# Performance work log

Hardware: AMD Instinct MI355X
Metric: run time of the kernel (lower is better)

The kernel has to match this reference:

```python
import math
import jax, jax.numpy as jnp
import numpy as np

T = 100        # temporal_scale
N = 32         # num_sample
PERBIN = 3     # num_sample_perbin
RATIO = 0.5    # prop_boundary_ratio
FEAT = 400     # feat_dim
B = 4          # batch


def _make_sample_mask(tscale=T, ratio=RATIO, n=N, perbin=PERBIN):
    # mask[t, sample_idx, start_idx, end_idx], faithful to _get_sample_mask
    mask = np.zeros((tscale, n, tscale, tscale), dtype=np.float64)
    for end_i in range(tscale):
        for start_i in range(end_i + 1):
            sp, ep = float(start_i), float(end_i + 1)
            L = ep - sp + 1.0
            sp2 = sp - L * ratio
            ep2 = ep + L * ratio
            step = (ep2 - sp2) / (n * perbin - 1.0)
            samples = [sp2 + step * i for i in range(n * perbin)]
            for i in range(n):
                for j in samples[i * perbin:(i + 1) * perbin]:
                    fr, it = math.modf(j)
                    it = int(it)
                    if 0 <= it < tscale - 1:
                        mask[it, i, start_i, end_i] += (1.0 - fr) / perbin
                        mask[it + 1, i, start_i, end_i] += fr / perbin
    return mask.reshape(tscale, -1).astype(np.float32)  # [T, N*T*T]


_DN = {1: ('NCH', 'OIH', 'NCH'), 2: ('NCHW', 'OIHW', 'NCHW'), 3: ('NCDHW', 'OIDHW', 'NCDHW')}


def _conv(x, w, b, stride, padding, groups=1):
    nd = x.ndim - 2
    if isinstance(stride, int):
        stride = (stride,) * nd
    if isinstance(padding, int):
        padding = [(padding, padding)] * nd
    y = jax.lax.conv_general_dilated(x, w, stride, padding,
                                     dimension_numbers=_DN[nd],
                                     feature_group_count=groups)
    return y + b.reshape((1, -1) + (1,) * nd)


def _forward(inputs, w_b1, b_b1, w_b2, b_b2, w_s1, b_s1, w_s2, b_s2,
             w_e1, b_e1, w_e2, b_e2, w_p1, b_p1, w3d, b3d,
             w2a, b2a, w2b, b2b, w2c, b2c, w2d, b2d, sample_mask):
    relu, sig = jax.nn.relu, jax.nn.sigmoid
    base = relu(_conv(inputs, w_b1, b_b1, 1, 1, 4))
    base = relu(_conv(base, w_b2, b_b2, 1, 1, 4))           # [B,256,T]
    start = sig(_conv(relu(_conv(base, w_s1, b_s1, 1, 1, 4)), w_s2, b_s2, 1, 0))[:, 0]
    end = sig(_conv(relu(_conv(base, w_e1, b_e1, 1, 1, 4)), w_e2, b_e2, 1, 0))[:, 0]
    p = relu(_conv(base, w_p1, b_p1, 1, 1))                 # [B,128,T]
    Bsz, C, Tt = p.shape
    n = w3d.shape[2]
    # boundary-matching layer: [B,128,T] @ [T, N*T*T] -> [B,128,N,T,T]
    bm = jnp.matmul(p, sample_mask).reshape(Bsz, C, n, Tt, Tt)
    bm = relu(_conv(bm, w3d, b3d, (n, 1, 1), 0))[:, :, 0]   # [B,512,T,T]
    x = relu(_conv(bm, w2a, b2a, 1, 0))
    x = relu(_conv(x, w2b, b2b, 1, 1))
    x = relu(_conv(x, w2c, b2c, 1, 1))
    conf = sig(_conv(x, w2d, b2d, 1, 0))                     # [B,2,T,T]
    return conf, start, end


def setup_inputs() -> dict:
    key = jax.random.key(0)
    ks = iter(jax.random.split(key, 40))

    def rn(shape, s=0.05):
        return jax.random.normal(next(ks), shape, jnp.float32) * s

    d = dict(
        inputs=jax.random.normal(next(ks), (B, FEAT, T), jnp.float32),
        w_b1=rn((256, FEAT // 4, 3)), b_b1=rn((256,)),
        w_b2=rn((256, 64, 3)), b_b2=rn((256,)),
        w_s1=rn((256, 64, 3)), b_s1=rn((256,)),
        w_s2=rn((1, 256, 1)), b_s2=rn((1,)),
        w_e1=rn((256, 64, 3)), b_e1=rn((256,)),
        w_e2=rn((1, 256, 1)), b_e2=rn((1,)),
        w_p1=rn((128, 256, 3)), b_p1=rn((128,)),
        w3d=rn((512, 128, N, 1, 1)), b3d=rn((512,)),
        w2a=rn((128, 512, 1, 1)), b2a=rn((128,)),
        w2b=rn((128, 128, 3, 3)), b2b=rn((128,)),
        w2c=rn((128, 128, 3, 3)), b2c=rn((128,)),
        w2d=rn((2, 128, 1, 1)), b2d=rn((2,)),
        sample_mask=jnp.asarray(_make_sample_mask()),
    )
    return d


def reference(inputs, w_b1, b_b1, w_b2, b_b2, w_s1, b_s1, w_s2, b_s2,
              w_e1, b_e1, w_e2, b_e2, w_p1, b_p1, w3d, b3d,
              w2a, b2a, w2b, b2b, w2c, b2c, w2d, b2d, sample_mask):
    return _forward(inputs, w_b1, b_b1, w_b2, b_b2, w_s1, b_s1, w_s2, b_s2,
                    w_e1, b_e1, w_e2, b_e2, w_p1, b_p1, w3d, b3d,
                    w2a, b2a, w2b, b2b, w2c, b2c, w2d, b2d, sample_mask)
```

## Files before the change

### kernel.cpp

```cpp
#include <hip/hip_runtime.h>
#include <cstdint>
#include <cstddef>
#include <math.h>

typedef unsigned short u16;
typedef short bf16x8 __attribute__((ext_vector_type(8)));
typedef float f32x4 __attribute__((ext_vector_type(4)));

__device__ __forceinline__ u16 f2bf(float f) {
  union { float f; uint32_t u; } c; c.f = f;
  uint32_t u = c.u;
  return (u16)((u + 0x7FFFu + ((u >> 16) & 1u)) >> 16);
}
__device__ __forceinline__ float bf2f(u16 h) {
  union { uint32_t u; float f; } c; c.u = ((uint32_t)h) << 16;
  return c.f;
}
__device__ __forceinline__ float sigmoidf_(float x) { return 1.f / (1.f + expf(-x)); }

__device__ __forceinline__ void glds16(const void* g, void* l) {
  __builtin_amdgcn_global_load_lds((const __attribute__((address_space(1))) void*)g,
                                   (__attribute__((address_space(3))) void*)l, 16, 0, 0);
}

__device__ __forceinline__ int col_rank(int p) {
  int s = p / 100, e = p - s * 100;
  int tri = (s * (s - 1)) >> 1;
  return (e >= s) ? (p - tri - s) : (5050 + tri + e);
}

__global__ void conv1d_k3v(const float* __restrict__ in, const float* __restrict__ w,
                           const float* __restrict__ bias, float* __restrict__ out,
                           int Cin_total, int Cin_g, int ocPerGroup, int OC) {
  int idx = blockIdx.x * 256 + threadIdx.x;
  int sub = idx % 25;
  int tmp = idx / 25;
  int oc = tmp % OC;
  int bb = tmp / OC;
  if (bb >= 4) return;
  int t4 = sub * 4;
  int g = oc / ocPerGroup;
  const float* ip = in + ((size_t)bb * Cin_total + (size_t)g * Cin_g) * 100 + t4;
  const float* wp = w + (size_t)oc * Cin_g * 3;
  float bs = bias[oc];
  float s0 = bs, s1 = bs, s2 = bs, s3 = bs;
  #pragma unroll 4
  for (int ic = 0; ic < Cin_g; ++ic) {
    const float* r = ip + (size_t)ic * 100;
    float4 a = *(const float4*)r;
    float xm = (t4 > 0) ? r[-1] : 0.f;
    float xp = (t4 < 96) ? r[4] : 0.f;
    float w0 = wp[ic * 3 + 0], w1 = wp[ic * 3 + 1], w2 = wp[ic * 3 + 2];
    s0 += w0 * xm + w1 * a.x + w2 * a.y;
    s1 += w0 * a.x + w1 * a.y + w2 * a.z;
    s2 += w0 * a.y + w1 * a.z + w2 * a.w;
    s3 += w0 * a.z + w1 * a.w + w2 * xp;
  }
  float4 o;
  o.x = fmaxf(s0, 0.f); o.y = fmaxf(s1, 0.f);
  o.z = fmaxf(s2, 0.f); o.w = fmaxf(s3, 0.f);
  *(float4*)(out + ((size_t)bb * OC + oc) * 100 + t4) = o;
}

__global__ void conv1d_branch_v(const float* __restrict__ in, const float* __restrict__ wS,
                                const float* __restrict__ bS, const float* __restrict__ wE,
                                const float* __restrict__ bE, const float* __restrict__ wP,
                                const float* __restrict__ bP, float* __restrict__ outS,
                                float* __restrict__ outE, u16* __restrict__ Pt) {
  int idx = blockIdx.x * 256 + threadIdx.x;
  int sub = idx % 25;
  int tmp = idx / 25;
  int ocx = tmp % 640;
  int bb = tmp / 640;
  if (bb >= 4) return;
  int t4 = sub * 4;
  const float* w;
  const float* bias;
  const float* ip;
  int Cin_g, oc;
  if (ocx < 512) {
    int sel = ocx >> 8;
    oc = ocx & 255;
    w = sel ? wE : wS;
    bias = sel ? bE : bS;
    int g = oc >> 6;
    ip = in + ((size_t)bb * 256 + (size_t)g * 64) * 100 + t4;
    Cin_g = 64;
  } else {
    oc = ocx - 512;
    w = wP;
    bias = bP;
    ip = in + (size_t)bb * 256 * 100 + t4;
    Cin_g = 256;
  }
  const float* wp = w + (size_t)oc * Cin_g * 3;
  float bs = bias[oc];
  float s0 = bs, s1 = bs, s2 = bs, s3 = bs;
  #pragma unroll 4
  for (int ic = 0; ic < Cin_g; ++ic) {
    const float* r = ip + (size_t)ic * 100;
    float4 a = *(const float4*)r;
    float xm = (t4 > 0) ? r[-1] : 0.f;
    float xp = (t4 < 96) ? r[4] : 0.f;
    float w0 = wp[ic * 3 + 0], w1 = wp[ic * 3 + 1], w2 = wp[ic * 3 + 2];
    s0 += w0 * xm + w1 * a.x + w2 * a.y;
    s1 += w0 * a.x + w1 * a.y + w2 * a.z;
    s2 += w0 * a.y + w1 * a.z + w2 * a.w;
    s3 += w0 * a.z + w1 * a.w + w2 * xp;
  }
  if (ocx < 512) {
    float* out = (ocx < 256) ? outS : outE;
    float4 o;
    o.x = fmaxf(s0, 0.f); o.y = fmaxf(s1, 0.f);
    o.z = fmaxf(s2, 0.f); o.w = fmaxf(s3, 0.f);
    *(float4*)(out + ((size_t)bb * 256 + oc) * 100 + t4) = o;
  } else {
    Pt[((size_t)bb * 100 + t4 + 0) * 128 + oc] = f2bf(fmaxf(s0, 0.f));
    Pt[((size_t)bb * 100 + t4 + 1) * 128 + oc] = f2bf(fmaxf(s1, 0.f));
    Pt[((size_t)bb * 100 + t4 + 2) * 128 + oc] = f2bf(fmaxf(s2, 0.f));
    Pt[((size_t)bb * 100 + t4 + 3) * 128 + oc] = f2bf(fmaxf(s3, 0.f));
  }
}

__global__ void prep_fused(const float* __restrict__ w2a, const float* __restrict__ w2b,
                           const float* __restrict__ w2c, u16* __restrict__ w2a_bf,
                           u16* __restrict__ w2b_pk, u16* __restrict__ w2c_pk,
                           const float* __restrict__ w3d, u16* __restrict__ Wq,
                           int* __restrict__ invperm, int* __restrict__ tinfo,
                           int* __restrict__ order, u16* __restrict__ zp,
                           u16* __restrict__ Mt, const float* __restrict__ inputs,
                           const float* __restrict__ w_b1, const float* __restrict__ b_b1,
                           float* __restrict__ base1) {
  __shared__ __align__(16) u16 ML[4 * 3200];
  __shared__ int C[128];
  int bid = blockIdx.x, tid = threadIdx.x;
  if (bid < 576) {
    int i = bid * 256 + tid;
    if (i < 65536) w2a_bf[i] = f2bf(w2a[i]);
    if (i < 147456) {
      int oc = i / 1152, r = i % 1152, kk = r >> 7, ic = r & 127;
      int src = (oc * 128 + ic) * 9 + kk;
      w2b_pk[i] = f2bf(w2b[src]);
      w2c_pk[i] = f2bf(w2c[src]);
    }
  } else if (bid < 640) {
    int u = (bid - 576) * 256 + tid;
    int o = u >> 5, n = u & 31;
    const float* src = w3d + (size_t)o * 4096 + n;
    u16* dst = Wq + (size_t)u * 128;
    for (int c0 = 0; c0 < 128; c0 += 8) {
      __align__(16) u16 h[8];
      #pragma unroll
      for (int j = 0; j < 8; ++j) h[j] = f2bf(src[(size_t)(c0 + j) * 32]);
      *(uint4*)(dst + c0) = *(const uint4*)h;
    }
  } else if (bid < 680) {
    int p = (bid - 640) * 256 + tid;
    if (p < 10000) invperm[col_rank(p)] = p;
  } else if (bid == 680) {
    if (tid < 128) zp[tid] = 0;
    int t = tid;
    int kbmin = 0, cnt = 0;
    if (t < 79) {
      int rlo = t * 128;
      int rhi = rlo + 128;
      if (rhi > 5050) rhi = 5050;
      if (rlo < 5050) {
        int s = 0;
        while (100 * (s + 1) - ((s + 1) * s) / 2 <= rlo) ++s;
        int cum = 100 * s - (s * (s - 1)) / 2;
        int tmin = 100, tmax = -1;
        for (int r = rlo; r < rhi; ++r) {
          while (r - cum >= 100 - s) { ++s; cum = 100 * s - (s * (s - 1)) / 2; }
          int e = s + (r - cum);
          float L = (float)(e - s + 2);
          float sp2 = (float)s - 0.5f * L;
          float ep2 = (float)(e + 1) + 0.5f * L;
          int a = (int)floorf(sp2) - 1;
          if (a < 0) a = 0;
          int b = (int)floorf(ep2) + 2;
          if (b > 99) b = 99;
          if (a < tmin) tmin = a;
          if (b > tmax) tmax = b;
        }
        kbmin = tmin >> 1;
        cnt = (tmax >> 1) - kbmin + 1;
      }
      tinfo[2 * t] = kbmin;
      tinfo[2 * t + 1] = cnt;
    }
    if (t < 128) C[t] = (t < 79) ? cnt : -1;
    __syncthreads();
    if (t < 79) {
      int pos = 0;
      int ct = C[t];
      for (int u = 0; u < 79; ++u) {
        int cu = C[u];
        pos += (cu > ct) || (cu == ct && u < t);
      }
      order[pos] = t;
    }
  } else if (bid < 1961) {
    int r0 = (bid - 681) * 4;
    uint32_t* MZ = (uint32_t*)ML;
    for (int i = tid; i < 6400; i += 256) MZ[i] = 0;
    __syncthreads();
    int g = tid >> 6, lane = tid & 63;
    int r = r0 + g;
    if (r < 5050 && lane < 32) {
      int n = lane;
      int s = (int)((201.0 - sqrt((double)(40401 - 8 * r))) * 0.5);
      if (s < 0) s = 0;
      while (s * (201 - s) / 2 > r) --s;
      while ((s + 1) * (200 - s) / 2 <= r) ++s;
      int e = s + (r - s * (201 - s) / 2);
      double sp = (double)s, ep = (double)(e + 1);
      double L = ep - sp + 1.0;
      double sp2 = sp - L * 0.5;
      double ep2 = ep + L * 0.5;
      double step = (ep2 - sp2) / 95.0;
      double win[8];
      #pragma unroll
      for (int k = 0; k < 8; ++k) win[k] = 0.0;
      int base = -1;
      #pragma unroll
      for (int jj = 0; jj < 3; ++jj) {
        double pos = sp2 + step * (double)(n * 3 + jj);
        double ip;
        double fr = modf(pos, &ip);
        int it = (int)ip;
        if (it >= 0 && it < 99) {
          if (base < 0) base = it;
          int off = it - base;
          win[off] += (1.0 - fr) / 3.0;
          win[off + 1] += fr / 3.0;
        }
      }
      if (base >= 0) {
        u16* dst = ML + g * 3200 + n;
        #pragma unroll
        for (int k = 0; k < 8; ++k) {
          int t = base + k;
          if (t < 100) dst[t * 32] = f2bf((float)win[k]);
        }
      }
    }
    __syncthreads();
    for (int i = tid; i < 1600; i += 256) {
      int rl = i / 400, off = i - rl * 400;
      *(uint4*)(Mt + (size_t)(r0 + rl) * 3200 + off * 8) = ((const uint4*)ML)[i];
    }
  } else {
    int idx = (bid - 1961) * 256 + tid;
    int sub = idx % 25;
    int tmp = idx / 25;
    int oc = tmp % 256;
    int bb = tmp / 256;
    if (bb >= 4) return;
    int t4 = sub * 4;
    int g = oc >> 6;
    const float* ip = inputs + ((size_t)bb * 400 + (size_t)g * 100) * 100 + t4;
    const float* wp = w_b1 + (size_t)oc * 300;
    float bs = b_b1[oc];
    float s0 = bs, s1 = bs, s2 = bs, s3 = bs;
    #pragma unroll 4
    for (int ic = 0; ic < 100; ++ic) {
      const float* rr = ip + (size_t)ic * 100;
      float4 a = *(const float4*)rr;
      float xm = (t4 > 0) ? rr[-1] : 0.f;
      float xp = (t4 < 96) ? rr[4] : 0.f;
      float w0 = wp[ic * 3 + 0], w1 = wp[ic * 3 + 1], w2 = wp[ic * 3 + 2];
      s0 += w0 * xm + w1 * a.x + w2 * a.y;
      s1 += w0 * a.x + w1 * a.y + w2 * a.z;
      s2 += w0 * a.y + w1 * a.z + w2 * a.w;
      s3 += w0 * a.z + w1 * a.w + w2 * xp;
    }
    float4 o;
    o.x = fmaxf(s0, 0.f); o.y = fmaxf(s1, 0.f);
    o.z = fmaxf(s2, 0.f); o.w = fmaxf(s3, 0.f);
    *(float4*)(base1 + ((size_t)bb * 256 + oc) * 100 + t4) = o;
  }
}

template<int MI>
__device__ __forceinline__ void mfma_stepT(const u16* As, const u16* Bs, int l, int wm, int wn,
                                           f32x4 (&acc)[MI][4]) {
  int m15 = l & 15, q = l >> 4, sw = m15 & 7;
  #pragma unroll
  for (int kk = 0; kk < 2; ++kk) {
    int koff = ((kk * 4 + q) ^ sw) * 8;
    bf16x8 av[MI], bv[4];
    #pragma unroll
    for (int i = 0; i < MI; ++i)
      av[i] = *(const bf16x8*)(As + (size_t)(wm * (MI * 16) + i * 16 + m15) * 64 + koff);
    #pragma unroll
    for (int j = 0; j < 4; ++j)
      bv[j] = *(const bf16x8*)(Bs + (size_t)(wn * 64 + j * 16 + m15) * 64 + koff);
    #pragma unroll
    for (int i = 0; i < MI; ++i) {
      #pragma unroll
      for (int j = 0; j < 4; ++j)
        acc[i][j] = __builtin_amdgcn_mfma_f32_16x16x32_bf16(av[i], bv[j], acc[i][j], 0, 0, 0);
    }
  }
}

template<int MI>
__device__ __forceinline__ void epilogue_storeT(f32x4 (&acc)[MI][4], u16* OUT,
                                                const float* bias, int row0, int col0, int l,
                                                int wm, int wn, int N, int OC, long long NPB,
                                                const int* colmap) {
  int r4 = (l >> 4) * 4, c1 = l & 15;
  int cols[4], pcols[4];
  #pragma unroll
  for (int j = 0; j < 4; ++j) {
    cols[j] = col0 + wn * 64 + j * 16 + c1;
    pcols[j] = (cols[j] < N) ? (colmap ? colmap[cols[j]] : cols[j]) : 0;
  }
  #pragma unroll
  for (int i = 0; i < MI; ++i) {
    int row = row0 + wm * (MI * 16) + i * 16 + r4;
    int ob = row % OC;
    size_t obb = (size_t)(row / OC) * (size_t)OC * (size_t)NPB;
    float b0 = bias[ob + 0], b1 = bias[ob + 1], b2 = bias[ob + 2], b3 = bias[ob + 3];
    #pragma unroll
    for (int j = 0; j < 4; ++j) {
      if (cols[j] < N) {
        f32x4 v = acc[i][j];
        __align__(8) u16 h[4];
        h[0] = f2bf(fmaxf(v[0] + b0, 0.f));
        h[1] = f2bf(fmaxf(v[1] + b1, 0.f));
        h[2] = f2bf(fmaxf(v[2] + b2, 0.f));
        h[3] = f2bf(fmaxf(v[3] + b3, 0.f));
        *(uint2*)(OUT + obb + (size_t)pcols[j] * OC + ob) = *(const uint2*)h;
      }
    }
  }
}

__global__ __launch_bounds__(256, 2) void gemm_bt(const u16* __restrict__ A,
                                                  const u16* __restrict__ B,
                                                  u16* __restrict__ OUT,
                                                  const float* __restrict__ bias, int N, int K,
                                                  const int* __restrict__ tinfo,
                                                  const int* __restrict__ order, int kblocks,
                                                  int OC, long long NPB, int NclampB,
                                                  const int* __restrict__ colmap) {
  __shared__ __align__(16) u16 As[128 * 64];
  __shared__ __align__(16) u16 Bs[128 * 64];
  int mt = blockIdx.x;
  int nt = order ? order[blockIdx.y] : blockIdx.y;
  int col0 = nt * 128, row0 = mt * 128;
  int tid = threadIdx.x, w = tid >> 6, l = tid & 63;
  int wm = w >> 1, wn = w & 1;
  int lr = l >> 3;
  int lk_sw = ((l & 7) ^ lr) * 8;
  f32x4 acc[4][4] = {};
  size_t aoff[4];
  size_t boff[4];
  #pragma unroll
  for (int r = 0; r < 4; ++r) {
    int chunk = r * 4 + w;
    int rowA = row0 + chunk * 8 + lr;
    aoff[r] = (size_t)rowA * K + lk_sw;
    int colB = col0 + chunk * 8 + lr;
    if (colB >= NclampB) colB = NclampB - 1;
    boff[r] = (size_t)colB * K + lk_sw;
  }
  int kbmin = 0, cnt = kblocks;
  if (tinfo) { kbmin = tinfo[2 * nt]; cnt = tinfo[2 * nt + 1]; }
  for (int i = 0; i < cnt; ++i) {
    int k0 = (kbmin + i) * 64;
    #pragma unroll
    for (int r = 0; r < 4; ++r) {
      int chunk = r * 4 + w;
      glds16(A + aoff[r] + k0, As + chunk * 512);
      glds16(B + boff[r] + k0, Bs + chunk * 512);
    }
    __syncthreads();
    mfma_stepT<4>(As, Bs, l, wm, wn, acc);
    __syncthreads();
  }
  epilogue_storeT<4>(acc, OUT, bias, row0, col0, l, wm, wn, N, OC, NPB, colmap);
}

__global__ __launch_bounds__(256, 2) void qprep_sig(const u16* __restrict__ Wq,
                                                    const u16* __restrict__ Pt,
                                                    u16* __restrict__ Qb,
                                                    const float* __restrict__ s1,
                                                    const float* __restrict__ e1,
                                                    const float* __restrict__ ws2,
                                                    const float* __restrict__ bs2,
                                                    const float* __restrict__ we2,
                                                    const float* __restrict__ be2,
                                                    float* __restrict__ out) {
  if (blockIdx.x == 128) {
    int t = threadIdx.x & 127;
    int sel = threadIdx.x >> 7;
    int bb = blockIdx.y;
    if (t >= 100) return;
    const float* in = sel ? e1 : s1;
    const float* w = sel ? we2 : ws2;
    float s = sel ? be2[0] : bs2[0];
    #pragma unroll 8
    for (int c = 0; c < 256; ++c) s += w[c] * in[((size_t)bb * 256 + c) * 100 + t];
    out[80000 + sel * 400 + bb * 100 + t] = sigmoidf_(s);
    return;
  }
  __shared__ __align__(16) u16 As[128 * 64];
  __shared__ __align__(16) u16 Bs[128 * 64];
  int mt = blockIdx.x, nt = blockIdx.y;
  int col0 = nt * 128, row0 = mt * 128;
  int tid = threadIdx.x, w = tid >> 6, l = tid & 63;
  int wm = w >> 1, wn = w & 1;
  int lr = l >> 3;
  int lk_sw = ((l & 7) ^ lr) * 8;
  f32x4 acc[4][4] = {};
  size_t aoff[4];
  size_t boff[4];
  #pragma unroll
  for (int r = 0; r < 4; ++r) {
    int chunk = r * 4 + w;
    int rowA = row0 + chunk * 8 + lr;
    aoff[r] = (size_t)rowA * 128 + lk_sw;
    int colB = col0 + chunk * 8 + lr;
    if (colB >= 400) colB = 399;
    boff[r] = (size_t)colB * 128 + lk_sw;
  }
  #pragma unroll
  for (int kb = 0; kb < 2; ++kb) {
    int k0 = kb * 64;
    #pragma unroll
    for (int r = 0; r < 4; ++r) {
      int chunk = r * 4 + w;
      glds16(Wq + aoff[r] + k0, As + chunk * 512);
      glds16(Pt + boff[r] + k0, Bs + chunk * 512);
    }
    __syncthreads();
    mfma_stepT<4>(As, Bs, l, wm, wn, acc);
    __syncthreads();
  }
  int r4 = (l >> 4) * 4, c1 = l & 15;
  #pragma unroll
  for (int i = 0; i < 4; ++i) {
    int row = row0 + wm * 64 + i * 16 + r4;
    int o = row >> 5, n = row & 31;
    #pragma unroll
    for (int j = 0; j < 4; ++j) {
      int col = col0 + wn * 64 + j * 16 + c1;
      if (col < 400) {
        int b = col / 100, t = col - b * 100;
        f32x4 v = acc[i][j];
        __align__(8) u16 h[4];
        h[0] = f2bf(v[0]);
        h[1] = f2bf(v[1]);
        h[2] = f2bf(v[2]);
        h[3] = f2bf(v[3]);
        *(uint2*)(Qb + ((size_t)(b * 512 + o)) * 3200 + t * 32 + n) = *(const uint2*)h;
      }
    }
  }
}

template<int FUSE>
__global__ __launch_bounds__(256, 2) void conv3x3_gemm(const u16* __restrict__ Apk,
                                                       const u16* __restrict__ X,
                                                       u16* __restrict__ OUT,
                                                       const float* __restrict__ bias,
                                                       const u16* __restrict__ zp,
                                                       const float* __restrict__ w2d,
                                                       const float* __restrict__ b2d,
                                                       float* __restrict__ out) {
  __shared__ __align__(16) u16 SH[2 * 128 * 64];
  u16* As = SH;
  u16* Bs = SH + 128 * 64;
  int nt = blockIdx.x;
  int col0 = nt * 128;
  int tid = threadIdx.x, w = tid >> 6, l = tid & 63;
  int wm = w >> 1, wn = w & 1;
  int lr = l >> 3;
  int lk_sw = ((l & 7) ^ lr) * 8;
  int cj[4], yy[4], xx[4];
  bool vv[4];
  size_t aoff[4];
  #pragma unroll
  for (int r = 0; r < 4; ++r) {
    int chunk = r * 4 + w;
    int c = col0 + chunk * 8 + lr;
    cj[r] = c;
    vv[r] = (c < 40000);
    int p = c % 10000;
    yy[r] = p / 100;
    xx[r] = p % 100;
    aoff[r] = (size_t)(chunk * 8 + lr) * 1152 + lk_sw;
  }
  f32x4 acc[4][4] = {};
  for (int s = 0; s < 9; ++s) {
    int dy = s / 3 - 1, dx = s % 3 - 1;
    int doff = dy * 100 + dx;
    #pragma unroll
    for (int half = 0; half < 2; ++half) {
      int k0 = s * 128 + half * 64;
      int c0 = half * 64;
      #pragma unroll
      for (int r = 0; r < 4; ++r) {
        int chunk = r * 4 + w;
        glds16(Apk + aoff[r] + k0, As + chunk * 512);
        int y2 = yy[r] + dy, x2 = xx[r] + dx;
        bool ok = vv[r] && ((unsigned)y2 < 100u) && ((unsigned)x2 < 100u);
        const u16* src = ok ? (X + (size_t)(cj[r] + doff) * 128 + c0 + lk_sw) : zp;
        glds16(src, Bs + chunk * 512);
      }
      __syncthreads();
      mfma_stepT<4>(As, Bs, l, wm, wn, acc);
      __syncthreads();
    }
  }
  if (FUSE == 0) {
    epilogue_storeT<4>(acc, OUT, bias, 0, col0, l, wm, wn, 40000, 128, 40000LL, nullptr);
  } else {
    uint32_t* W = (uint32_t*)SH;
    int r4 = (l >> 4) * 4, c1 = l & 15;
    #pragma unroll
    for (int i = 0; i < 4; ++i) {
      int ob = wm * 64 + i * 16 + r4;
      float b0 = bias[ob + 0], b1 = bias[ob + 1], b2 = bias[ob + 2], b3 = bias[ob + 3];
      #pragma unroll
      for (int j = 0; j < 4; ++j) {
        int col = wn * 64 + j * 16 + c1;
        f32x4 v = acc[i][j];
        uint32_t lo = (uint32_t)f2bf(fmaxf(v[0] + b0, 0.f)) |
                      ((uint32_t)f2bf(fmaxf(v[1] + b1, 0.f)) << 16);
        uint32_t hi = (uint32_t)f2bf(fmaxf(v[2] + b2, 0.f)) |
                      ((uint32_t)f2bf(fmaxf(v[3] + b3, 0.f)) << 16);
        int jj = ob >> 1;
        W[col * 64 + (jj ^ (col & 31))] = lo;
        W[col * 64 + ((jj + 1) ^ (col & 31))] = hi;
      }
    }
    __syncthreads();
    int col = tid & 127, sel = tid >> 7;
    int gcol = col0 + col;
    if (gcol < 40000) {
      float sum = b2d[sel];
      const uint32_t* Wc = W + col * 64;
      const float* wd = w2d + sel * 128;
      #pragma unroll 8
      for (int c = 0; c < 64; ++c) {
        uint32_t v = Wc[c ^ (col & 31)];
        sum += wd[2 * c] * bf2f((u16)(v & 0xffffu)) + wd[2 * c + 1] * bf2f((u16)(v >> 16));
      }
      int b = gcol / 10000, pidx = gcol - b * 10000;
      out[((size_t)b * 2 + sel) * 10000 + pidx] = sigmoidf_(sum);
    }
  }
}

extern "C" void kernel_launch(void* const* d_in, const int* in_sizes, int n_in, void* d_out,
                              int out_size, void* d_ws, size_t ws_size, hipStream_t stream) {
  const float* inputs = (const float*)d_in[0];
  const float* w_b1 = (const float*)d_in[1];
  const float* b_b1 = (const float*)d_in[2];
  const float* w_b2 = (const float*)d_in[3];
  const float* b_b2 = (const float*)d_in[4];
  const float* w_s1 = (const float*)d_in[5];
  const float* b_s1 = (const float*)d_in[6];
  const float* w_s2 = (const float*)d_in[7];
  const float* b_s2 = (const float*)d_in[8];
  const float* w_e1 = (const float*)d_in[9];
  const float* b_e1 = (const float*)d_in[10];
  const float* w_e2 = (const float*)d_in[11];
  const float* b_e2 = (const float*)d_in[12];
  const float* w_p1 = (const float*)d_in[13];
  const float* b_p1 = (const float*)d_in[14];
  const float* w3d = (const float*)d_in[15];
  const float* b3d = (const float*)d_in[16];
  const float* w2a = (const float*)d_in[17];
  const float* b2a = (const float*)d_in[18];
  const float* w2b = (const float*)d_in[19];
  const float* b2b = (const float*)d_in[20];
  const float* w2c = (const float*)d_in[21];
  const float* b2c = (const float*)d_in[22];
  const float* w2d = (const float*)d_in[23];
  const float* b2d = (const float*)d_in[24];
  float* out = (float*)d_out;
  char* ws = (char*)d_ws;

  int* tinfo = (int*)(ws + 0);
  int* order = (int*)(ws + 2048);
  u16* zp = (u16*)(ws + 16384);
  int* invperm = (int*)(ws + 45056);
  float* base1 = (float*)(ws + 90112);
  float* base = (float*)(ws + 499712);
  float* s1buf = (float*)(ws + 909312);
  u16* Pt = (u16*)(ws + 1318912);
  u16* w2a_bf = (u16*)(ws + 1421312);
  u16* w2b_pk = (u16*)(ws + 1552384);
  u16* w2c_pk = (u16*)(ws + 1847296);
  u16* Qb = (u16*)(ws + 2142208);
  u16* Mt = (u16*)(ws + 15249408);
  float* e1buf = (float*)(ws + 48017408);
  u16* C1t = (u16*)(ws + 79249408);
  u16* Wq = (u16*)(ws + 79249408);
  u16* x2t = Qb;
  u16* x3t = C1t;

  prep_fused<<<2061, 256, 0, stream>>>(w2a, w2b, w2c, w2a_bf, w2b_pk, w2c_pk, w3d, Wq,
                                       invperm, tinfo, order, zp, Mt, inputs, w_b1, b_b1,
                                       base1);

  conv1d_k3v<<<100, 256, 0, stream>>>(base1, w_b2, b_b2, base, 256, 64, 64, 256);
  conv1d_branch_v<<<250, 256, 0, stream>>>(base, w_s1, b_s1, w_e1, b_e1, w_p1, b_p1,
                                           s1buf, e1buf, Pt);

  qprep_sig<<<dim3(129, 4), 256, 0, stream>>>(Wq, Pt, Qb, s1buf, e1buf, w_s2, b_s2,
                                              w_e2, b_e2, out);

  gemm_bt<<<dim3(16, 79), 256, 0, stream>>>(Qb, Mt, C1t, b3d, 10000, 3200, tinfo, order, 50,
                                            512, 10000LL, 10000, invperm);
  gemm_bt<<<dim3(1, 313), 256, 0, stream>>>(w2a_bf, C1t, x2t, b2a, 40000, 512, nullptr,
                                            nullptr, 8, 128, 40000LL, 40000, nullptr);
  conv3x3_gemm<0><<<dim3(313), 256, 0, stream>>>(w2b_pk, x2t, x3t, b2b, zp, nullptr, nullptr,
                                                 nullptr);
  conv3x3_gemm<1><<<dim3(313), 256, 0, stream>>>(w2c_pk, x3t, nullptr, b2c, zp, w2d, b2d,
                                                 out);
}
```

Measured before the change: 257.4 us.

## Split conv1d input channels across 4 lanes and coalesce GEMM epilogue stores via LDS

The three 1D conv kernels now split each output's input-channel reduction across 4 adjacent lanes and combine the partial sums with xor shuffles. This gives 4x more threads and shorter serial loops, raising parallelism for these small, latency-bound kernels. Separately, the GEMM and conv3x3 epilogue now stage bf16 results in shared memory and write each output column as contiguous 16-byte stores instead of scattered 8-byte stores. The costs are an extra __syncthreads, LDS traffic and shuffle reductions.

```diff
diff --git a/kernel.cpp b/kernel.cpp
--- a/kernel.cpp
+++ b/kernel.cpp
@@ -29,96 +29,105 @@
   return (e >= s) ? (p - tri - s) : (5050 + tri + e);
 }
 
-__global__ void conv1d_k3v(const float* __restrict__ in, const float* __restrict__ w,
-                           const float* __restrict__ bias, float* __restrict__ out,
-                           int Cin_total, int Cin_g, int ocPerGroup, int OC) {
-  int idx = blockIdx.x * 256 + threadIdx.x;
-  int sub = idx % 25;
-  int tmp = idx / 25;
-  int oc = tmp % OC;
-  int bb = tmp / OC;
-  if (bb >= 4) return;
+__global__ void conv2_r(const float* __restrict__ in, const float* __restrict__ w,
+                        const float* __restrict__ bias, float* __restrict__ out) {
+  int u = blockIdx.x * 256 + threadIdx.x;
+  int r = u & 3;
+  int quad = u >> 2;
+  int sub = quad % 25;
+  int tmp = quad / 25;
+  int oc = tmp & 255;
+  int bb = tmp >> 8;
   int t4 = sub * 4;
-  int g = oc / ocPerGroup;
-  const float* ip = in + ((size_t)bb * Cin_total + (size_t)g * Cin_g) * 100 + t4;
-  const float* wp = w + (size_t)oc * Cin_g * 3;
-  float bs = bias[oc];
-  float s0 = bs, s1 = bs, s2 = bs, s3 = bs;
+  int g = oc >> 6;
+  const float* ip = in + ((size_t)bb * 256 + g * 64 + r * 16) * 100 + t4;
+  const float* wp = w + (size_t)oc * 192 + r * 48;
+  float s0 = 0.f, s1 = 0.f, s2 = 0.f, s3 = 0.f;
   #pragma unroll 4
-  for (int ic = 0; ic < Cin_g; ++ic) {
-    const float* r = ip + (size_t)ic * 100;
-    float4 a = *(const float4*)r;
-    float xm = (t4 > 0) ? r[-1] : 0.f;
-    float xp = (t4 < 96) ? r[4] : 0.f;
-    float w0 = wp[ic * 3 + 0], w1 = wp[ic * 3 + 1], w2 = wp[ic * 3 + 2];
+  for (int i = 0; i < 16; ++i) {
+    const float* rr = ip + (size_t)i * 100;
+    float4 a = *(const float4*)rr;
+    float xm = (t4 > 0) ? rr[-1] : 0.f;
+    float xp = (t4 < 96) ? rr[4] : 0.f;
+    float w0 = wp[i * 3 + 0], w1 = wp[i * 3 + 1], w2 = wp[i * 3 + 2];
     s0 += w0 * xm + w1 * a.x + w2 * a.y;
     s1 += w0 * a.x + w1 * a.y + w2 * a.z;
     s2 += w0 * a.y + w1 * a.z + w2 * a.w;
     s3 += w0 * a.z + w1 * a.w + w2 * xp;
   }
-  float4 o;
-  o.x = fmaxf(s0, 0.f); o.y = fmaxf(s1, 0.f);
-  o.z = fmaxf(s2, 0.f); o.w = fmaxf(s3, 0.f);
-  *(float4*)(out + ((size_t)bb * OC + oc) * 100 + t4) = o;
-}
-
-__global__ void conv1d_branch_v(const float* __restrict__ in, const float* __restrict__ wS,
-                                const float* __restrict__ bS, const float* __restrict__ wE,
-                                const float* __restrict__ bE, const float* __restrict__ wP,
-                                const float* __restrict__ bP, float* __restrict__ outS,
-                                float* __restrict__ outE, u16* __restrict__ Pt) {
-  int idx = blockIdx.x * 256 + threadIdx.x;
-  int sub = idx % 25;
-  int tmp = idx / 25;
+  s0 += __shfl_xor(s0, 1); s0 += __shfl_xor(s0, 2);
+  s1 += __shfl_xor(s1, 1); s1 += __shfl_xor(s1, 2);
+  s2 += __shfl_xor(s2, 1); s2 += __shfl_xor(s2, 2);
+  s3 += __shfl_xor(s3, 1); s3 += __shfl_xor(s3, 2);
+  if (r == 0) {
+    float b = bias[oc];
+    float4 o;
+    o.x = fmaxf(s0 + b, 0.f); o.y = fmaxf(s1 + b, 0.f);
+    o.z = fmaxf(s2 + b, 0.f); o.w = fmaxf(s3 + b, 0.f);
+    *(float4*)(out + ((size_t)bb * 256 + oc) * 100 + t4) = o;
+  }
+}
+
+__global__ void branch_r(const float* __restrict__ in, const float* __restrict__ wS,
+                         const float* __restrict__ bS, const float* __restrict__ wE,
+                         const float* __restrict__ bE, const float* __restrict__ wP,
+                         const float* __restrict__ bP, float* __restrict__ outS,
+                         float* __restrict__ outE, u16* __restrict__ Pt) {
+  int u = blockIdx.x * 256 + threadIdx.x;
+  int r = u & 3;
+  int quad = u >> 2;
+  int sub = quad % 25;
+  int tmp = quad / 25;
   int ocx = tmp % 640;
   int bb = tmp / 640;
-  if (bb >= 4) return;
   int t4 = sub * 4;
-  const float* w;
-  const float* bias;
+  const float* wp;
   const float* ip;
-  int Cin_g, oc;
+  int oc, iters;
   if (ocx < 512) {
     int sel = ocx >> 8;
     oc = ocx & 255;
-    w = sel ? wE : wS;
-    bias = sel ? bE : bS;
+    wp = (sel ? wE : wS) + (size_t)oc * 192 + r * 48;
     int g = oc >> 6;
-    ip = in + ((size_t)bb * 256 + (size_t)g * 64) * 100 + t4;
-    Cin_g = 64;
+    ip = in + ((size_t)bb * 256 + g * 64 + r * 16) * 100 + t4;
+    iters = 16;
   } else {
     oc = ocx - 512;
-    w = wP;
-    bias = bP;
-    ip = in + (size_t)bb * 256 * 100 + t4;
-    Cin_g = 256;
-  }
-  const float* wp = w + (size_t)oc * Cin_g * 3;
-  float bs = bias[oc];
-  float s0 = bs, s1 = bs, s2 = bs, s3 = bs;
-  #pragma unroll 4
-  for (int ic = 0; ic < Cin_g; ++ic) {
-    const float* r = ip + (size_t)ic * 100;
-    float4 a = *(const float4*)r;
-    float xm = (t4 > 0) ? r[-1] : 0.f;
-    float xp = (t4 < 96) ? r[4] : 0.f;
-    float w0 = wp[ic * 3 + 0], w1 = wp[ic * 3 + 1], w2 = wp[ic * 3 + 2];
+    wp = wP + (size_t)oc * 768 + r * 192;
+    ip = in + ((size_t)bb * 256 + r * 64) * 100 + t4;
+    iters = 64;
+  }
+  float s0 = 0.f, s1 = 0.f, s2 = 0.f, s3 = 0.f;
+  for (int i = 0; i < iters; ++i) {
+    const float* rr = ip + (size_t)i * 100;
+    float4 a = *(const float4*)rr;
+    float xm = (t4 > 0) ? rr[-1] : 0.f;
+    float xp = (t4 < 96) ? rr[4] : 0.f;
+    float w0 = wp[i * 3 + 0], w1 = wp[i * 3 + 1], w2 = wp[i * 3 + 2];
     s0 += w0 * xm + w1 * a.x + w2 * a.y;
     s1 += w0 * a.x + w1 * a.y + w2 * a.z;
     s2 += w0 * a.y + w1 * a.z + w2 * a.w;
     s3 += w0 * a.z + w1 * a.w + w2 * xp;
   }
-  if (ocx < 512) {
-    float* out = (ocx < 256) ? outS : outE;
-    float4 o;
-    o.x = fmaxf(s0, 0.f); o.y = fmaxf(s1, 0.f);
-    o.z = fmaxf(s2, 0.f); o.w = fmaxf(s3, 0.f);
-    *(float4*)(out + ((size_t)bb * 256 + oc) * 100 + t4) = o;
-  } else {
-    Pt[((size_t)bb * 100 + t4 + 0) * 128 + oc] = f2bf(fmaxf(s0, 0.f));
-    Pt[((size_t)bb * 100 + t4 + 1) * 128 + oc] = f2bf(fmaxf(s1, 0.f));
-    Pt[((size_t)bb * 100 + t4 + 2) * 128 + oc] = f2bf(fmaxf(s2, 0.f));
-    Pt[((size_t)bb * 100 + t4 + 3) * 128 + oc] = f2bf(fmaxf(s3, 0.f));
+  s0 += __shfl_xor(s0, 1); s0 += __shfl_xor(s0, 2);
+  s1 += __shfl_xor(s1, 1); s1 += __shfl_xor(s1, 2);
+  s2 += __shfl_xor(s2, 1); s2 += __shfl_xor(s2, 2);
+  s3 += __shfl_xor(s3, 1); s3 += __shfl_xor(s3, 2);
+  if (r == 0) {
+    if (ocx < 512) {
+      float b = (ocx < 256) ? bS[oc] : bE[oc];
+      float* out = (ocx < 256) ? outS : outE;
+      float4 o;
+      o.x = fmaxf(s0 + b, 0.f); o.y = fmaxf(s1 + b, 0.f);
+      o.z = fmaxf(s2 + b, 0.f); o.w = fmaxf(s3 + b, 0.f);
+      *(float4*)(out + ((size_t)bb * 256 + oc) * 100 + t4) = o;
+    } else {
+      float b = bP[oc];
+      Pt[((size_t)bb * 100 + t4 + 0) * 128 + oc] = f2bf(fmaxf(s0 + b, 0.f));
+      Pt[((size_t)bb * 100 + t4 + 1) * 128 + oc] = f2bf(fmaxf(s1 + b, 0.f));
+      Pt[((size_t)bb * 100 + t4 + 2) * 128 + oc] = f2bf(fmaxf(s2 + b, 0.f));
+      Pt[((size_t)bb * 100 + t4 + 3) * 128 + oc] = f2bf(fmaxf(s3 + b, 0.f));
+    }
   }
 }
 
@@ -251,34 +260,41 @@
       *(uint4*)(Mt + (size_t)(r0 + rl) * 3200 + off * 8) = ((const uint4*)ML)[i];
     }
   } else {
-    int idx = (bid - 1961) * 256 + tid;
-    int sub = idx % 25;
-    int tmp = idx / 25;
-    int oc = tmp % 256;
-    int bb = tmp / 256;
-    if (bb >= 4) return;
+    int u = (bid - 1961) * 256 + tid;
+    int r = u & 3;
+    int quad = u >> 2;
+    int sub = quad % 25;
+    int tmp = quad / 25;
+    int oc = tmp & 255;
+    int bb = tmp >> 8;
     int t4 = sub * 4;
     int g = oc >> 6;
-    const float* ip = inputs + ((size_t)bb * 400 + (size_t)g * 100) * 100 + t4;
-    const float* wp = w_b1 + (size_t)oc * 300;
-    float bs = b_b1[oc];
-    float s0 = bs, s1 = bs, s2 = bs, s3 = bs;
-    #pragma unroll 4
-    for (int ic = 0; ic < 100; ++ic) {
-      const float* rr = ip + (size_t)ic * 100;
+    const float* ip = inputs + ((size_t)bb * 400 + g * 100 + r * 25) * 100 + t4;
+    const float* wp = w_b1 + (size_t)oc * 300 + r * 75;
+    float s0 = 0.f, s1 = 0.f, s2 = 0.f, s3 = 0.f;
+    #pragma unroll 5
+    for (int i = 0; i < 25; ++i) {
+      const float* rr = ip + (size_t)i * 100;
       float4 a = *(const float4*)rr;
       float xm = (t4 > 0) ? rr[-1] : 0.f;
       float xp = (t4 < 96) ? rr[4] : 0.f;
-      float w0 = wp[ic * 3 + 0], w1 = wp[ic * 3 + 1], w2 = wp[ic * 3 + 2];
+      float w0 = wp[i * 3 + 0], w1 = wp[i * 3 + 1], w2 = wp[i * 3 + 2];
       s0 += w0 * xm + w1 * a.x + w2 * a.y;
       s1 += w0 * a.x + w1 * a.y + w2 * a.z;
       s2 += w0 * a.y + w1 * a.z + w2 * a.w;
       s3 += w0 * a.z + w1 * a.w + w2 * xp;
     }
-    float4 o;
-    o.x = fmaxf(s0, 0.f); o.y = fmaxf(s1, 0.f);
-    o.z = fmaxf(s2, 0.f); o.w = fmaxf(s3, 0.f);
-    *(float4*)(base1 + ((size_t)bb * 256 + oc) * 100 + t4) = o;
+    s0 += __shfl_xor(s0, 1); s0 += __shfl_xor(s0, 2);
+    s1 += __shfl_xor(s1, 1); s1 += __shfl_xor(s1, 2);
+    s2 += __shfl_xor(s2, 1); s2 += __shfl_xor(s2, 2);
+    s3 += __shfl_xor(s3, 1); s3 += __shfl_xor(s3, 2);
+    if (r == 0) {
+      float b = b_b1[oc];
+      float4 o;
+      o.x = fmaxf(s0 + b, 0.f); o.y = fmaxf(s1 + b, 0.f);
+      o.z = fmaxf(s2 + b, 0.f); o.w = fmaxf(s3 + b, 0.f);
+      *(float4*)(base1 + ((size_t)bb * 256 + oc) * 100 + t4) = o;
+    }
   }
 }
 
@@ -305,36 +321,44 @@
   }
 }
 
-template<int MI>
-__device__ __forceinline__ void epilogue_storeT(f32x4 (&acc)[MI][4], u16* OUT,
-                                                const float* bias, int row0, int col0, int l,
-                                                int wm, int wn, int N, int OC, long long NPB,
-                                                const int* colmap) {
+__device__ __forceinline__ void epilogue_coal(f32x4 (&acc)[4][4], u16* SH, u16* OUT,
+                                              const float* bias, int row0, int col0, int tid,
+                                              int l, int wm, int wn, int N, int OC,
+                                              long long NPB, const int* colmap) {
+  uint32_t* W = (uint32_t*)SH;
   int r4 = (l >> 4) * 4, c1 = l & 15;
-  int cols[4], pcols[4];
+  int bb0 = row0 % OC;
   #pragma unroll
-  for (int j = 0; j < 4; ++j) {
-    cols[j] = col0 + wn * 64 + j * 16 + c1;
-    pcols[j] = (cols[j] < N) ? (colmap ? colmap[cols[j]] : cols[j]) : 0;
-  }
-  #pragma unroll
-  for (int i = 0; i < MI; ++i) {
-    int row = row0 + wm * (MI * 16) + i * 16 + r4;
-    int ob = row % OC;
-    size_t obb = (size_t)(row / OC) * (size_t)OC * (size_t)NPB;
-    float b0 = bias[ob + 0], b1 = bias[ob + 1], b2 = bias[ob + 2], b3 = bias[ob + 3];
+  for (int i = 0; i < 4; ++i) {
+    int ob = wm * 64 + i * 16 + r4;
+    float b0 = bias[bb0 + ob + 0], b1 = bias[bb0 + ob + 1];
+    float b2 = bias[bb0 + ob + 2], b3 = bias[bb0 + ob + 3];
+    int jj = ob >> 1;
     #pragma unroll
     for (int j = 0; j < 4; ++j) {
-      if (cols[j] < N) {
-        f32x4 v = acc[i][j];
-        __align__(8) u16 h[4];
-        h[0] = f2bf(fmaxf(v[0] + b0, 0.f));
-        h[1] = f2bf(fmaxf(v[1] + b1, 0.f));
-        h[2] = f2bf(fmaxf(v[2] + b2, 0.f));
-        h[3] = f2bf(fmaxf(v[3] + b3, 0.f));
-        *(uint2*)(OUT + obb + (size_t)pcols[j] * OC + ob) = *(const uint2*)h;
-      }
-    }
+      int col = wn * 64 + j * 16 + c1;
+      f32x4 v = acc[i][j];
+      uint32_t lo = (uint32_t)f2bf(fmaxf(v[0] + b0, 0.f)) |
+                    ((uint32_t)f2bf(fmaxf(v[1] + b1, 0.f)) << 16);
+      uint32_t hi = (uint32_t)f2bf(fmaxf(v[2] + b2, 0.f)) |
+                    ((uint32_t)f2bf(fmaxf(v[3] + b3, 0.f)) << 16);
+      W[col * 64 + (jj ^ (col & 31))] = lo;
+      W[col * 64 + ((jj + 1) ^ (col & 31))] = hi;
+    }
+  }
+  __syncthreads();
+  int col = tid >> 1, half = tid & 1;
+  int gcol = col0 + col;
+  if (gcol < N) {
+    int pcol = colmap ? colmap[gcol] : gcol;
+    const uint32_t* Wc = W + col * 64;
+    __align__(16) uint32_t tbuf[32];
+    #pragma unroll
+    for (int k = 0; k < 32; ++k) tbuf[k] = Wc[(half * 32 + k) ^ (col & 31)];
+    u16* dst = OUT + (size_t)(row0 / OC) * (size_t)OC * (size_t)NPB + (size_t)pcol * OC +
+               bb0 + half * 64;
+    #pragma unroll
+    for (int q = 0; q < 8; ++q) *(uint4*)(dst + q * 8) = *(const uint4*)(tbuf + q * 4);
   }
 }
 
@@ -346,8 +370,9 @@
                                                   const int* __restrict__ order, int kblocks,
                                                   int OC, long long NPB, int NclampB,
                                                   const int* __restrict__ colmap) {
-  __shared__ __align__(16) u16 As[128 * 64];
-  __shared__ __align__(16) u16 Bs[128 * 64];
+  __shared__ __align__(16) u16 SH[2 * 128 * 64];
+  u16* As = SH;
+  u16* Bs = SH + 128 * 64;
   int mt = blockIdx.x;
   int nt = order ? order[blockIdx.y] : blockIdx.y;
   int col0 = nt * 128, row0 = mt * 128;
@@ -381,7 +406,7 @@
     mfma_stepT<4>(As, Bs, l, wm, wn, acc);
     __syncthreads();
   }
-  epilogue_storeT<4>(acc, OUT, bias, row0, col0, l, wm, wn, N, OC, NPB, colmap);
+  epilogue_coal(acc, SH, OUT, bias, row0, col0, tid, l, wm, wn, N, OC, NPB, colmap);
 }
 
 __global__ __launch_bounds__(256, 2) void qprep_sig(const u16* __restrict__ Wq,
@@ -517,7 +542,7 @@
     }
   }
   if (FUSE == 0) {
-    epilogue_storeT<4>(acc, OUT, bias, 0, col0, l, wm, wn, 40000, 128, 40000LL, nullptr);
+    epilogue_coal(acc, SH, OUT, bias, 0, col0, tid, l, wm, wn, 40000, 128, 40000LL, nullptr);
   } else {
     uint32_t* W = (uint32_t*)SH;
     int r4 = (l >> 4) * 4, c1 = l & 15;
@@ -605,13 +630,13 @@
   u16* x2t = Qb;
   u16* x3t = C1t;
 
-  prep_fused<<<2061, 256, 0, stream>>>(w2a, w2b, w2c, w2a_bf, w2b_pk, w2c_pk, w3d, Wq,
+  prep_fused<<<2361, 256, 0, stream>>>(w2a, w2b, w2c, w2a_bf, w2b_pk, w2c_pk, w3d, Wq,
                                        invperm, tinfo, order, zp, Mt, inputs, w_b1, b_b1,
                                        base1);
 
-  conv1d_k3v<<<100, 256, 0, stream>>>(base1, w_b2, b_b2, base, 256, 64, 64, 256);
-  conv1d_branch_v<<<250, 256, 0, stream>>>(base, w_s1, b_s1, w_e1, b_e1, w_p1, b_p1,
-                                           s1buf, e1buf, Pt);
+  conv2_r<<<400, 256, 0, stream>>>(base1, w_b2, b_b2, base);
+  branch_r<<<1000, 256, 0, stream>>>(base, w_s1, b_s1, w_e1, b_e1, w_p1, b_p1,
+                                     s1buf, e1buf, Pt);
 
   qprep_sig<<<dim3(129, 4), 256, 0, stream>>>(Wq, Pt, Qb, s1buf, e1buf, w_s2, b_s2,
                                               w_e2, b_e2, out);
```

New measurement: 267.5 us. 3.9% more time.
